# Kernel optimization log

Hardware: AMD Instinct MI355X
Metric: run time of the kernel (lower is better)

The kernel has to match this reference:

```python
import jax, jax.numpy as jnp
import numpy as np


def setup_inputs() -> dict:
    key = jax.random.key(0)
    k1, k2, k3 = jax.random.split(key, 3)
    x = jax.random.normal(k1, (32, 256, 32, 32), dtype=jnp.float32)
    weight = jax.random.normal(k2, (256, 256, 3, 3), dtype=jnp.float32) * 0.05
    bias = jax.random.normal(k3, (256,), dtype=jnp.float32) * 0.01
    return {"x": x, "weight": weight, "bias": bias}


def _forward(x, weight, bias):
    B, cin, n, _ = x.shape
    cout, _, k, _ = weight.shape
    s = (k - 1) // 2
    nf = n // 2 + 1
    bins = n * nf

    # fft shift matrix: exp(-1j*2*pi*s*(i+j)/n), kept rfft columns
    idx = jnp.arange(n)
    shift = idx[None, :] + idx[:, None]                     # (n, n)
    shift_m = jnp.exp(-1j * 2 * jnp.pi * s * shift / n)[:, :nf]
    shift_m = shift_m.reshape(bins, 1, 1).astype(jnp.complex64)

    # xfft: (B, cin, n, nf) -> (bins, cin, B)
    xfft = jnp.fft.rfft2(x)
    xfft = jnp.transpose(xfft, (2, 3, 1, 0)).reshape(bins, cin, B)

    # Hfft: (cout, cin, n, nf) -> (bins, cout, cin), shifted + conj
    Hfft = jnp.fft.rfft2(weight, s=(n, n)).reshape(cout, cin, bins)
    Hfft = shift_m * jnp.conj(jnp.transpose(Hfft, (2, 0, 1)))

    def sq_abs(z):
        return jnp.real(z) ** 2 + jnp.imag(z) ** 2

    RowNorm = jnp.sqrt(jnp.sum(sq_abs(Hfft), axis=2))       # (bins, cout)
    ColNorm = jnp.sqrt(jnp.sum(sq_abs(Hfft), axis=1))       # (bins, cin)

    if cout >= cin:
        RowLoss = jnp.mean((RowNorm - jnp.sqrt(cin / cout)) ** 2)
        ColLoss = jnp.mean((ColNorm - 1.0) ** 2)
        HHT = jnp.einsum('npc,nqc->npq', jnp.conj(Hfft), Hfft)  # (bins, cout, cout)
        mask = jnp.triu(jnp.ones((cout, cout), bool), k=1)
        count = bins * (cout * (cout - 1) // 2)
        AngLoss = jnp.sum(sq_abs(HHT) * mask[None]) / count   # MSE(|HHT[triu]|, 0)
        L = cout * ColLoss + cin * RowLoss + AngLoss
    else:
        RowLoss = jnp.mean((RowNorm - 1.0) ** 2)
        ColLoss = jnp.mean((ColNorm - jnp.sqrt(cout / cin)) ** 2)
        HTH = jnp.einsum('ndp,ndq->npq', jnp.conj(Hfft), Hfft)  # (bins, cin, cin)
        mask = jnp.triu(jnp.ones((cin, cin), bool), k=1)
        count = bins * (cin * (cin - 1) // 2)
        AngLoss = jnp.sum(sq_abs(HTH) * mask[None]) / count
        L = cout * ColLoss + cin * RowLoss + AngLoss

    # per-bin complex matmul: (bins, cout, cin) @ (bins, cin, B) -> (bins, cout, B)
    yfft = Hfft @ xfft
    yfft = jnp.transpose(yfft.reshape(n, nf, cout, B), (3, 2, 0, 1))  # (B, cout, n, nf)
    y = jnp.fft.irfft2(yfft, s=(n, n))
    y = y + bias[None, :, None, None]
    return y, L


def reference(x, weight, bias):
    return _forward(x, weight, bias)
```

## Files before the change

kernel.cpp:

```cpp
#include <hip/hip_runtime.h>
#include <math.h>

typedef __attribute__((ext_vector_type(8)))  short  short8;
typedef __attribute__((ext_vector_type(16))) float  float16;

#define TWO_PI_OVER_32 0.19634954084936207f

static __device__ __forceinline__ unsigned short f2bf(float f) {
    unsigned int u = __float_as_uint(f);
    u = (u + 0x7FFFu + ((u >> 16) & 1u)) >> 16;
    return (unsigned short)u;
}
static __device__ __forceinline__ float bf2f(unsigned short s) {
    return __uint_as_float(((unsigned int)s) << 16);
}

static __device__ __forceinline__ void g2l16(const void* g, void* l) {
    __builtin_amdgcn_global_load_lds(
        (const __attribute__((address_space(1))) unsigned int*)g,
        (__attribute__((address_space(3))) unsigned int*)l, 16, 0, 0);
}

__global__ __launch_bounds__(256) void k_prepx(const float* __restrict__ x,
                                               unsigned short* __restrict__ xb,
                                               const float* __restrict__ w,
                                               unsigned short* __restrict__ wt,
                                               unsigned short* __restrict__ Vb,
                                               float* __restrict__ Drow,
                                               float* __restrict__ Dcol,
                                               float* __restrict__ accum) {
    int tid = threadIdx.x;
    if (blockIdx.x < 4096) {
        int g = blockIdx.x * 256 + tid;
        int c = g & 31, r = (g >> 5) & 31, cig = (g >> 10) & 31, b = g >> 15;
        const float* xp = x + ((b * 256 + cig * 8) * 32 + r) * 32 + c;
        union { unsigned short u[8]; uint4 v; } pk;
        #pragma unroll
        for (int u = 0; u < 8; ++u) pk.u[u] = f2bf(xp[u * 1024]);
        ((uint4*)xb)[g] = pk.v;
        return;
    }
    __shared__ float sdata[45];
    __shared__ float ws2[256 * 9];
    int blk = blockIdx.x - 4096, lane = tid & 63;
    bool colmode = blk >= 256;
    int pc = blk & 255;
    if (blk == 0 && tid < 4) accum[tid] = 0.f;
    if (tid < 45) sdata[tid] = 0.f;

    int p = colmode ? tid : pc;
    int c = colmode ? pc : tid;
    float w9[9];
    #pragma unroll
    for (int t = 0; t < 9; ++t) w9[t] = w[(p * 256 + c) * 9 + t];
    if (!colmode) {
        #pragma unroll
        for (int t = 0; t < 9; ++t) ws2[tid * 9 + t] = w9[t];
    }
    __syncthreads();

    int idx = 0;
    for (int ta = 0; ta < 9; ++ta)
        for (int tb = ta; tb < 9; ++tb) {
            float v = w9[ta] * w9[tb];
            #pragma unroll
            for (int off = 32; off > 0; off >>= 1) v += __shfl_down(v, off);
            if (lane == 0) atomicAdd(&sdata[idx], v);
            ++idx;
        }
    __syncthreads();
    if (tid < 45) (colmode ? Dcol : Drow)[pc * 45 + tid] = sdata[tid];

    if (!colmode) {
        #pragma unroll
        for (int t = 0; t < 9; ++t)
            wt[t * 65536 + (c >> 3) * 2048 + p * 8 + (c & 7)] = f2bf(w9[t]);
        if (tid < 320) {
            int ta = tid >> 5, cig = tid & 31;
            union { unsigned short u[8]; uint4 v; } pk;
            #pragma unroll
            for (int u = 0; u < 8; ++u)
                pk.u[u] = (ta < 9) ? f2bf(ws2[(cig * 8 + u) * 9 + ta]) : (unsigned short)0;
            ((uint4*)Vb)[(p * 10 + ta) * 32 + cig] = pk.v;
        }
    }
}

__global__ __launch_bounds__(256, 2) void k_conv(const unsigned short* __restrict__ xb,
                                                 const unsigned short* __restrict__ wt,
                                                 const float* __restrict__ bias,
                                                 float* __restrict__ y) {
    __shared__ unsigned short xs[2][640 * 8];
    __shared__ unsigned short wsm[2][1152 * 8];

    const int tid  = threadIdx.x;
    const int lane = tid & 63;
    const int wv   = tid >> 6;
    const int half = lane >> 5;
    const int m    = lane & 31;

    const int id    = blockIdx.x;
    const int xcd   = id & 7;
    const int local = id >> 3;
    const int b     = xcd * 4 + (local >> 4);
    const int rem   = local & 15;
    const int co0   = (rem & 3) * 64;
    const int r0    = (rem >> 2) * 8;

    float16 acc[2][2];
    #pragma unroll
    for (int i = 0; i < 2; ++i)
        #pragma unroll
        for (int ns = 0; ns < 2; ++ns)
            #pragma unroll
            for (int r = 0; r < 16; ++r) acc[i][ns][r] = 0.f;

    const uint4* xbv = (const uint4*)xb;
    const uint4* wtv = (const uint4*)wt;

    const int cigl = lane >> 5;
    const int coll = lane & 31;

    auto stage = [&](int buf, int kc) {
        uint4* xd = (uint4*)xs[buf];
        uint4* wd = (uint4*)wsm[buf];
        #pragma unroll
        for (int ch = wv; ch < 28; ch += 4) {
            if (ch < 10) {
                int gr = (r0 + ch + 31) & 31;
                g2l16(&xbv[((b * 32 + kc * 2 + cigl) * 32 + gr) * 32 + coll],
                      &xd[ch * 64]);
            } else {
                int wc = ch - 10;
                int t = wc >> 1, cig = wc & 1;
                g2l16(&wtv[t * 8192 + (kc * 2 + cig) * 256 + co0 + lane],
                      &wd[wc * 64]);
            }
        }
    };

    auto compute = [&](int buf) {
        const short8* xsl = (const short8*)xs[buf];
        const short8* wsl = (const short8*)wsm[buf];
        #pragma unroll
        for (int t = 0; t < 9; ++t) {
            const int atv = t / 3, btv = t % 3;
            short8 a0 = wsl[(t * 2 + half) * 64 + m];
            short8 a1 = wsl[(t * 2 + half) * 64 + 32 + m];
            #pragma unroll
            for (int ns = 0; ns < 2; ++ns) {
                int slot = wv * 2 + ns + atv;
                short8 bf = xsl[(slot * 2 + half) * 32 + ((m + btv + 31) & 31)];
                acc[0][ns] = __builtin_amdgcn_mfma_f32_32x32x16_bf16(a0, bf, acc[0][ns], 0, 0, 0);
                acc[1][ns] = __builtin_amdgcn_mfma_f32_32x32x16_bf16(a1, bf, acc[1][ns], 0, 0, 0);
            }
        }
    };

    stage(0, 0);
    #pragma unroll 1
    for (int kc2 = 0; kc2 < 8; ++kc2) {
        __syncthreads();
        stage(1, 2 * kc2 + 1);
        compute(0);
        __syncthreads();
        if (kc2 < 7) stage(0, 2 * kc2 + 2);
        compute(1);
    }

    #pragma unroll
    for (int i = 0; i < 2; ++i) {
        #pragma unroll
        for (int ns = 0; ns < 2; ++ns) {
            int r = r0 + wv * 2 + ns;
            #pragma unroll
            for (int reg = 0; reg < 16; ++reg) {
                int crow = (reg & 3) + 8 * (reg >> 2) + 4 * half;
                int co = co0 + i * 32 + crow;
                y[(b * 256 + co) * 1024 + r * 32 + m] = acc[i][ns][reg] + bias[co];
            }
        }
    }
}

__global__ __launch_bounds__(256) void k_gram(const unsigned short* __restrict__ Vb,
                                              unsigned short* __restrict__ Gb) {
    int blk = blockIdx.x, I = 0;
    while (blk >= 20 - I) { blk -= 20 - I; ++I; }
    int J = I + blk;

    const int tid  = threadIdx.x;
    const int lane = tid & 63;
    const int wave = tid >> 6;
    const int wm = wave >> 1, wn = wave & 1;
    const int half = lane >> 5;
    const int m = lane & 31;

    const int row0 = I * 128 + wm * 64;
    const int col0 = J * 128 + wn * 64;

    float16 acc[2][2];
    #pragma unroll
    for (int i = 0; i < 2; ++i)
        #pragma unroll
        for (int j = 0; j < 2; ++j)
            #pragma unroll
            for (int r = 0; r < 16; ++r) acc[i][j][r] = 0.f;

    const short8* vb = (const short8*)Vb;
    for (int kc = 0; kc < 16; ++kc) {
        int cig = kc * 2 + half;
        short8 a0 = vb[(row0 + m) * 32 + cig];
        short8 a1 = vb[(row0 + 32 + m) * 32 + cig];
        short8 b0 = vb[(col0 + m) * 32 + cig];
        short8 b1 = vb[(col0 + 32 + m) * 32 + cig];
        acc[0][0] = __builtin_amdgcn_mfma_f32_32x32x16_bf16(a0, b0, acc[0][0], 0, 0, 0);
        acc[0][1] = __builtin_amdgcn_mfma_f32_32x32x16_bf16(a0, b1, acc[0][1], 0, 0, 0);
        acc[1][0] = __builtin_amdgcn_mfma_f32_32x32x16_bf16(a1, b0, acc[1][0], 0, 0, 0);
        acc[1][1] = __builtin_amdgcn_mfma_f32_32x32x16_bf16(a1, b1, acc[1][1], 0, 0, 0);
    }
    #pragma unroll
    for (int i = 0; i < 2; ++i)
        #pragma unroll
        for (int j = 0; j < 2; ++j)
            #pragma unroll
            for (int reg = 0; reg < 16; ++reg) {
                int crow = (reg & 3) + 8 * (reg >> 2) + 4 * half;
                Gb[(row0 + i * 32 + crow) * 2560 + col0 + j * 32 + m] =
                    f2bf(acc[i][j][reg]);
            }
}

__global__ __launch_bounds__(256) void k_loss(const float* __restrict__ Drow,
                                              const float* __restrict__ Dcol,
                                              const unsigned short* __restrict__ Gb,
                                              float* __restrict__ accum) {
    __shared__ union {
        struct { float coef[45]; float red[2]; } rc;
        struct { unsigned short gs[9 * 2560]; float red; } ang;
    } sh;
    int tid = threadIdx.x;

    if (blockIdx.x < 544) {
        int bin = blockIdx.x;
        int u = bin / 17, v = bin % 17;
        if (tid < 2) sh.rc.red[tid] = 0.f;
        if (tid < 45) {
            int idx = 0, TA = 0, TB = 0;
            for (int ta = 0; ta < 9; ++ta)
                for (int tb = ta; tb < 9; ++tb) {
                    if (idx == tid) { TA = ta; TB = tb; }
                    ++idx;
                }
            int da = TA / 3 - TB / 3;
            int db = TA % 3 - TB % 3;
            float cth = cosf(TWO_PI_OVER_32 * (float)(u * da + v * db));
            sh.rc.coef[tid] = (TA == TB) ? 1.f : 2.f * cth;
        }
        __syncthreads();

        float s1 = 0.f, s2 = 0.f;
        const float* dr = Drow + tid * 45;
        const float* dc = Dcol + tid * 45;
        #pragma unroll
        for (int i = 0; i < 45; ++i) {
            s1 += sh.rc.coef[i] * dr[i];
            s2 += sh.rc.coef[i] * dc[i];
        }
        float e1 = sqrtf(fmaxf(s1, 0.f)) - 1.f; e1 *= e1;
        float e2 = sqrtf(fmaxf(s2, 0.f)) - 1.f; e2 *= e2;
        #pragma unroll
        for (int off = 32; off > 0; off >>= 1) {
            e1 += __shfl_down(e1, off);
            e2 += __shfl_down(e2, off);
        }
        if ((tid & 63) == 0) { atomicAdd(&sh.rc.red[0], e1); atomicAdd(&sh.rc.red[1], e2); }
        __syncthreads();
        if (tid == 0) { atomicAdd(&accum[0], sh.rc.red[0]); atomicAdd(&accum[1], sh.rc.red[1]); }
    } else {
        int p = blockIdx.x - 544;
        if (tid == 0) sh.ang.red = 0.f;
        uint4* gsv = (uint4*)sh.ang.gs;
        const uint4* gbv = (const uint4*)Gb;
        for (int i = tid; i < 2880; i += 256) {
            int rr = i / 320, cc = i - rr * 320;
            gsv[i] = gbv[(p * 10 + rr) * 320 + cc];
        }
        __syncthreads();

        int q = tid;
        float S = 0.f;
        if (q > p) {
            float g5[5][5];
            #pragma unroll
            for (int i = 0; i < 5; ++i)
                #pragma unroll
                for (int j = 0; j < 5; ++j) g5[i][j] = 0.f;
            #pragma unroll
            for (int ta = 0; ta < 9; ++ta)
                #pragma unroll
                for (int tb = 0; tb < 9; ++tb) {
                    float c = bf2f(sh.ang.gs[ta * 2560 + q * 10 + tb]);
                    g5[ta / 3 - tb / 3 + 2][ta % 3 - tb % 3 + 2] += c;
                }
            float ReS[5];
            #pragma unroll
            for (int d = 0; d < 5; ++d) {
                float s = 0.f;
                for (int vv = 0; vv < 17; ++vv)
                    s += cosf(TWO_PI_OVER_32 * (float)(vv * d));
                ReS[d] = s;
            }
            #pragma unroll
            for (int da = 0; da < 5; ++da)
                #pragma unroll
                for (int d1 = 0; d1 < 5; ++d1)
                    #pragma unroll
                    for (int d2 = 0; d2 < 5; ++d2) {
                        int dd = d1 - d2; if (dd < 0) dd = -dd;
                        S += g5[da][d1] * g5[da][d2] * ReS[dd];
                    }
            S *= 32.f;
        }
        #pragma unroll
        for (int off = 32; off > 0; off >>= 1) S += __shfl_down(S, off);
        if ((tid & 63) == 0) atomicAdd(&sh.ang.red, S);
        __syncthreads();
        if (tid == 0) atomicAdd(&accum[2], sh.ang.red);
    }
}

__global__ void k_fin(const float* __restrict__ accum, float* __restrict__ out) {
    if (threadIdx.x == 0 && blockIdx.x == 0) {
        float row = accum[0], col = accum[1], ang = accum[2];
        out[8388608] = row / 544.f + col / 544.f + ang / (544.f * 32640.f);
    }
}

extern "C" void kernel_launch(void* const* d_in, const int* in_sizes, int n_in,
                              void* d_out, int out_size, void* d_ws, size_t ws_size,
                              hipStream_t stream) {
    const float* x    = (const float*)d_in[0];
    const float* w    = (const float*)d_in[1];
    const float* bias = (const float*)d_in[2];
    float* out = (float*)d_out;

    char* ws = (char*)d_ws;
    unsigned short* wt = (unsigned short*)ws;
    unsigned short* xb = (unsigned short*)(ws + 1179648);
    unsigned short* Gb = xb;
    unsigned short* Vb = (unsigned short*)(ws + 17956864);
    float* Drow  = (float*)(ws + 19267584);
    float* Dcol  = (float*)(ws + 19313664);
    float* accum = (float*)(ws + 19359744);

    k_prepx <<<4608, 256, 0, stream>>>(x, xb, w, wt, Vb, Drow, Dcol, accum);
    k_conv  <<<512, 256, 0, stream>>>(xb, wt, bias, out);
    k_gram  <<<210, 256, 0, stream>>>(Vb, Gb);
    k_loss  <<<800, 256, 0, stream>>>(Drow, Dcol, Gb, accum);
    k_fin   <<<1, 64, 0, stream>>>(accum, out);
}
```

Before: 179.1 us.

## Fuse gram into conv launch, fold finalize into loss, simplify angular sum

The gram-matrix blocks now run as 210 extra blocks of the conv kernel, so they fill idle CUs alongside the conv tiles instead of needing their own launch. Gb moves to a separate workspace region because it can no longer alias xb while conv is still reading it. The finalize kernel is replaced by a last-block-done atomic counter inside k_loss. The per-thread cosine table and 125-term triple loop are replaced by a closed-form sum of squares and cross terms. Together these remove two kernel launches. The counter at accum[3] relies on being zeroed by prepx, which is not shown.

```diff
diff --git a/kernel.cpp b/kernel.cpp
--- a/kernel.cpp
+++ b/kernel.cpp
@@ -89,16 +89,60 @@
 __global__ __launch_bounds__(256, 2) void k_conv(const unsigned short* __restrict__ xb,
                                                  const unsigned short* __restrict__ wt,
                                                  const float* __restrict__ bias,
+                                                 const unsigned short* __restrict__ Vb,
+                                                 unsigned short* __restrict__ Gb,
                                                  float* __restrict__ y) {
     __shared__ unsigned short xs[2][640 * 8];
     __shared__ unsigned short wsm[2][1152 * 8];
 
     const int tid  = threadIdx.x;
     const int lane = tid & 63;
-    const int wv   = tid >> 6;
     const int half = lane >> 5;
     const int m    = lane & 31;
 
+    if (blockIdx.x >= 512) {
+        int blk = blockIdx.x - 512, I = 0;
+        while (blk >= 20 - I) { blk -= 20 - I; ++I; }
+        int J = I + blk;
+        const int wave = tid >> 6;
+        const int wm = wave >> 1, wn = wave & 1;
+        const int row0 = I * 128 + wm * 64;
+        const int col0 = J * 128 + wn * 64;
+
+        float16 acc[2][2];
+        #pragma unroll
+        for (int i = 0; i < 2; ++i)
+            #pragma unroll
+            for (int j = 0; j < 2; ++j)
+                #pragma unroll
+                for (int r = 0; r < 16; ++r) acc[i][j][r] = 0.f;
+
+        const short8* vb = (const short8*)Vb;
+        for (int kc = 0; kc < 16; ++kc) {
+            int cig = kc * 2 + half;
+            short8 a0 = vb[(row0 + m) * 32 + cig];
+            short8 a1 = vb[(row0 + 32 + m) * 32 + cig];
+            short8 b0 = vb[(col0 + m) * 32 + cig];
+            short8 b1 = vb[(col0 + 32 + m) * 32 + cig];
+            acc[0][0] = __builtin_amdgcn_mfma_f32_32x32x16_bf16(a0, b0, acc[0][0], 0, 0, 0);
+            acc[0][1] = __builtin_amdgcn_mfma_f32_32x32x16_bf16(a0, b1, acc[0][1], 0, 0, 0);
+            acc[1][0] = __builtin_amdgcn_mfma_f32_32x32x16_bf16(a1, b0, acc[1][0], 0, 0, 0);
+            acc[1][1] = __builtin_amdgcn_mfma_f32_32x32x16_bf16(a1, b1, acc[1][1], 0, 0, 0);
+        }
+        #pragma unroll
+        for (int i = 0; i < 2; ++i)
+            #pragma unroll
+            for (int j = 0; j < 2; ++j)
+                #pragma unroll
+                for (int reg = 0; reg < 16; ++reg) {
+                    int crow = (reg & 3) + 8 * (reg >> 2) + 4 * half;
+                    Gb[(row0 + i * 32 + crow) * 2560 + col0 + j * 32 + m] =
+                        f2bf(acc[i][j][reg]);
+                }
+        return;
+    }
+
+    const int wv   = tid >> 6;
     const int id    = blockIdx.x;
     const int xcd   = id & 7;
     const int local = id >> 3;
@@ -183,58 +227,11 @@
     }
 }
 
-__global__ __launch_bounds__(256) void k_gram(const unsigned short* __restrict__ Vb,
-                                              unsigned short* __restrict__ Gb) {
-    int blk = blockIdx.x, I = 0;
-    while (blk >= 20 - I) { blk -= 20 - I; ++I; }
-    int J = I + blk;
-
-    const int tid  = threadIdx.x;
-    const int lane = tid & 63;
-    const int wave = tid >> 6;
-    const int wm = wave >> 1, wn = wave & 1;
-    const int half = lane >> 5;
-    const int m = lane & 31;
-
-    const int row0 = I * 128 + wm * 64;
-    const int col0 = J * 128 + wn * 64;
-
-    float16 acc[2][2];
-    #pragma unroll
-    for (int i = 0; i < 2; ++i)
-        #pragma unroll
-        for (int j = 0; j < 2; ++j)
-            #pragma unroll
-            for (int r = 0; r < 16; ++r) acc[i][j][r] = 0.f;
-
-    const short8* vb = (const short8*)Vb;
-    for (int kc = 0; kc < 16; ++kc) {
-        int cig = kc * 2 + half;
-        short8 a0 = vb[(row0 + m) * 32 + cig];
-        short8 a1 = vb[(row0 + 32 + m) * 32 + cig];
-        short8 b0 = vb[(col0 + m) * 32 + cig];
-        short8 b1 = vb[(col0 + 32 + m) * 32 + cig];
-        acc[0][0] = __builtin_amdgcn_mfma_f32_32x32x16_bf16(a0, b0, acc[0][0], 0, 0, 0);
-        acc[0][1] = __builtin_amdgcn_mfma_f32_32x32x16_bf16(a0, b1, acc[0][1], 0, 0, 0);
-        acc[1][0] = __builtin_amdgcn_mfma_f32_32x32x16_bf16(a1, b0, acc[1][0], 0, 0, 0);
-        acc[1][1] = __builtin_amdgcn_mfma_f32_32x32x16_bf16(a1, b1, acc[1][1], 0, 0, 0);
-    }
-    #pragma unroll
-    for (int i = 0; i < 2; ++i)
-        #pragma unroll
-        for (int j = 0; j < 2; ++j)
-            #pragma unroll
-            for (int reg = 0; reg < 16; ++reg) {
-                int crow = (reg & 3) + 8 * (reg >> 2) + 4 * half;
-                Gb[(row0 + i * 32 + crow) * 2560 + col0 + j * 32 + m] =
-                    f2bf(acc[i][j][reg]);
-            }
-}
-
 __global__ __launch_bounds__(256) void k_loss(const float* __restrict__ Drow,
                                               const float* __restrict__ Dcol,
                                               const unsigned short* __restrict__ Gb,
-                                              float* __restrict__ accum) {
+                                              float* __restrict__ accum,
+                                              float* __restrict__ out) {
     __shared__ union {
         struct { float coef[45]; float red[2]; } rc;
         struct { unsigned short gs[9 * 2560]; float red; } ang;
@@ -303,23 +300,13 @@
                     float c = bf2f(sh.ang.gs[ta * 2560 + q * 10 + tb]);
                     g5[ta / 3 - tb / 3 + 2][ta % 3 - tb % 3 + 2] += c;
                 }
-            float ReS[5];
-            #pragma unroll
-            for (int d = 0; d < 5; ++d) {
-                float s = 0.f;
-                for (int vv = 0; vv < 17; ++vv)
-                    s += cosf(TWO_PI_OVER_32 * (float)(vv * d));
-                ReS[d] = s;
+            #pragma unroll
+            for (int da = 0; da < 5; ++da) {
+                const float* g = g5[da];
+                float sq = g[0]*g[0] + g[1]*g[1] + g[2]*g[2] + g[3]*g[3] + g[4]*g[4];
+                float cr = g[0]*g[2] + g[1]*g[3] + g[2]*g[4] + g[0]*g[4];
+                S += 17.f * sq + 2.f * cr;
             }
-            #pragma unroll
-            for (int da = 0; da < 5; ++da)
-                #pragma unroll
-                for (int d1 = 0; d1 < 5; ++d1)
-                    #pragma unroll
-                    for (int d2 = 0; d2 < 5; ++d2) {
-                        int dd = d1 - d2; if (dd < 0) dd = -dd;
-                        S += g5[da][d1] * g5[da][d2] * ReS[dd];
-                    }
             S *= 32.f;
         }
         #pragma unroll
@@ -328,12 +315,16 @@
         __syncthreads();
         if (tid == 0) atomicAdd(&accum[2], sh.ang.red);
     }
-}
-
-__global__ void k_fin(const float* __restrict__ accum, float* __restrict__ out) {
-    if (threadIdx.x == 0 && blockIdx.x == 0) {
-        float row = accum[0], col = accum[1], ang = accum[2];
-        out[8388608] = row / 544.f + col / 544.f + ang / (544.f * 32640.f);
+
+    __threadfence();
+    if (tid == 0) {
+        unsigned int old = atomicAdd((unsigned int*)(accum + 3), 1u);
+        if (old == 799u) {
+            float row = atomicAdd(&accum[0], 0.f);
+            float col = atomicAdd(&accum[1], 0.f);
+            float ang = atomicAdd(&accum[2], 0.f);
+            out[8388608] = row / 544.f + col / 544.f + ang / (544.f * 32640.f);
+        }
     }
 }
 
@@ -348,15 +339,13 @@
     char* ws = (char*)d_ws;
     unsigned short* wt = (unsigned short*)ws;
     unsigned short* xb = (unsigned short*)(ws + 1179648);
-    unsigned short* Gb = xb;
     unsigned short* Vb = (unsigned short*)(ws + 17956864);
     float* Drow  = (float*)(ws + 19267584);
     float* Dcol  = (float*)(ws + 19313664);
     float* accum = (float*)(ws + 19359744);
+    unsigned short* Gb = (unsigned short*)(ws + 19392512);
 
     k_prepx <<<4608, 256, 0, stream>>>(x, xb, w, wt, Vb, Drow, Dcol, accum);
-    k_conv  <<<512, 256, 0, stream>>>(xb, wt, bias, out);
-    k_gram  <<<210, 256, 0, stream>>>(Vb, Gb);
-    k_loss  <<<800, 256, 0, stream>>>(Drow, Dcol, Gb, accum);
-    k_fin   <<<1, 64, 0, stream>>>(accum, out);
-}
+    k_conv  <<<722, 256, 0, stream>>>(xb, wt, bias, Vb, Gb, out);
+    k_loss  <<<800, 256, 0, stream>>>(Drow, Dcol, Gb, accum, out);
+}
```

After: 219.8 us. 1.23x slower.
